# Optimization experiments

Hardware: AMD Instinct MI355X
Metric: run time of the kernel (lower is better)

## Reference

```python
import jax, jax.numpy as jnp
import numpy as np

ITERATIONS = 20
EPS = 1e-9

def setup_inputs() -> dict:
    key = jax.random.key(0)
    x = jax.random.normal(key, (8192, 64, 64), dtype=jnp.float32)
    return {"x": x}

def reference(x):
    M = jnp.exp(x)
    def body(_, M):
        M = M / (jnp.sum(M, axis=-1, keepdims=True) + EPS)
        M = M / (jnp.sum(M, axis=-2, keepdims=True) + EPS)
        return M
    M = jax.lax.fori_loop(0, ITERATIONS, body, M)
    return M
```

## Files before the change

kernel.cpp:

```cpp
#include <hip/hip_runtime.h>

#define ITERS 20
#define EPS 1e-9f

typedef float v2f __attribute__((ext_vector_type(2)));


template <int CTRL>
__device__ __forceinline__ float dpp_add(float x) {
    int yi = __builtin_amdgcn_update_dpp(0, __float_as_int(x), CTRL, 0xf, 0xf, true);
    return x + __int_as_float(yi);
}

#if __has_builtin(__builtin_amdgcn_permlane16_swap)
__device__ __forceinline__ float xadd16(float x) {
    unsigned u = __float_as_uint(x);
    auto r = __builtin_amdgcn_permlane16_swap(u, u, false, false);
    return __uint_as_float(r[0]) + __uint_as_float(r[1]);
}
#else
__device__ __forceinline__ float xadd16(float x) {
    return x + __int_as_float(__builtin_amdgcn_ds_swizzle(__float_as_int(x), 0x401F));
}
#endif

#if __has_builtin(__builtin_amdgcn_permlane32_swap)
__device__ __forceinline__ float xadd32(float x) {
    unsigned u = __float_as_uint(x);
    auto r = __builtin_amdgcn_permlane32_swap(u, u, false, false);
    return __uint_as_float(r[0]) + __uint_as_float(r[1]);
}
#else
__device__ __forceinline__ float xadd32(float x) {
    return x + __shfl_xor(x, 32, 64);
}
#endif

__device__ __forceinline__ v2f pk_mul(v2f a, v2f b) {
    v2f d;
    asm("v_pk_mul_f32 %0, %1, %2" : "=v"(d) : "v"(a), "v"(b));
    return d;
}
__device__ __forceinline__ v2f pk_fma(v2f a, v2f b, v2f c) {
    v2f d;
    asm("v_pk_fma_f32 %0, %1, %2, %3" : "=v"(d) : "v"(a), "v"(b), "v"(c));
    return d;
}
__device__ __forceinline__ v2f pk_add(v2f a, v2f b) {
    v2f d;
    asm("v_pk_add_f32 %0, %1, %2" : "=v"(d) : "v"(a), "v"(b));
    return d;
}
__device__ __forceinline__ v2f pk_fma_bl(v2f a, v2f u2, v2f c) {
    v2f d;
    asm("v_pk_fma_f32 %0, %1, %2, %3 op_sel:[0,0,0] op_sel_hi:[1,0,1]"
        : "=v"(d) : "v"(a), "v"(u2), "v"(c));
    return d;
}
__device__ __forceinline__ v2f pk_fma_bh(v2f a, v2f u2, v2f c) {
    v2f d;
    asm("v_pk_fma_f32 %0, %1, %2, %3 op_sel:[0,1,0] op_sel_hi:[1,1,1]"
        : "=v"(d) : "v"(a), "v"(u2), "v"(c));
    return d;
}
__device__ __forceinline__ v2f pk_mul_bl(v2f a, v2f u2) {
    v2f d;
    asm("v_pk_mul_f32 %0, %1, %2 op_sel:[0,0] op_sel_hi:[1,0]"
        : "=v"(d) : "v"(a), "v"(u2));
    return d;
}
__device__ __forceinline__ v2f pk_mul_bh(v2f a, v2f u2) {
    v2f d;
    asm("v_pk_mul_f32 %0, %1, %2 op_sel:[0,1] op_sel_hi:[1,1]"
        : "=v"(d) : "v"(a), "v"(u2));
    return d;
}

__global__ __launch_bounds__(256, 2) void sinkhorn_kernel(
        const float* __restrict__ x, float* __restrict__ out, int nmat) {
    const int lane = threadIdx.x & 63;
    const int wave = threadIdx.x >> 6;
    const int mat  = blockIdx.x * 4 + wave;
    if (mat >= nmat) return;
    const int bi = lane >> 3;
    const int bj = lane & 7;

    const float4* __restrict__ xin = (const float4*)(x + (size_t)mat * 4096);

    v2f b2[8][4];
    #pragma unroll
    for (int r = 0; r < 8; ++r) {
        float4 lo = xin[(8 * bi + r) * 16 + 2 * bj + 0];
        float4 hi = xin[(8 * bi + r) * 16 + 2 * bj + 1];
        b2[r][0] = (v2f){__expf(lo.x), __expf(lo.y)};
        b2[r][1] = (v2f){__expf(lo.z), __expf(lo.w)};
        b2[r][2] = (v2f){__expf(hi.x), __expf(hi.y)};
        b2[r][3] = (v2f){__expf(hi.z), __expf(hi.w)};
    }

    v2f uu2[4], vv2[4];
    #pragma unroll
    for (int i = 0; i < 4; ++i) {
        uu2[i] = (v2f){1.0f, 1.0f};
        vv2[i] = (v2f){1.0f, 1.0f};
    }

    for (int it = 0; it < ITERS; ++it) {
        float p[8];
        #pragma unroll
        for (int r = 0; r < 8; ++r) {
            v2f s2 = pk_mul(b2[r][0], vv2[0]);
            s2 = pk_fma(b2[r][1], vv2[1], s2);
            s2 = pk_fma(b2[r][2], vv2[2], s2);
            s2 = pk_fma(b2[r][3], vv2[3], s2);
            p[r] = s2.x + s2.y;
        }
        #pragma unroll
        for (int r = 0; r < 8; ++r) p[r] = dpp_add<0xB1>(p[r]);
        #pragma unroll
        for (int r = 0; r < 8; ++r) p[r] = dpp_add<0x4E>(p[r]);
        #pragma unroll
        for (int r = 0; r < 8; ++r) p[r] = dpp_add<0x141>(p[r]);
        #pragma unroll
        for (int k = 0; k < 4; ++k) {
            uu2[k].x = __builtin_amdgcn_rcpf(p[2 * k + 0] + EPS);
            uu2[k].y = __builtin_amdgcn_rcpf(p[2 * k + 1] + EPS);
        }

        v2f qe[4], qo[4];
        #pragma unroll
        for (int c = 0; c < 4; ++c) {
            qe[c] = pk_mul_bl(b2[0][c], uu2[0]);
            qo[c] = pk_mul_bh(b2[1][c], uu2[0]);
        }
        #pragma unroll
        for (int k = 1; k < 4; ++k) {
            #pragma unroll
            for (int c = 0; c < 4; ++c) {
                qe[c] = pk_fma_bl(b2[2 * k + 0][c], uu2[k], qe[c]);
                qo[c] = pk_fma_bh(b2[2 * k + 1][c], uu2[k], qo[c]);
            }
        }
        float q[8];
        #pragma unroll
        for (int c = 0; c < 4; ++c) {
            v2f s2 = pk_add(qe[c], qo[c]);
            q[2 * c + 0] = s2.x;
            q[2 * c + 1] = s2.y;
        }
        #pragma unroll
        for (int c = 0; c < 8; ++c) q[c] = dpp_add<0x128>(q[c]);
        #pragma unroll
        for (int c = 0; c < 8; ++c) q[c] = xadd16(q[c]);
        #pragma unroll
        for (int c = 0; c < 8; ++c) q[c] = xadd32(q[c]);
        #pragma unroll
        for (int c = 0; c < 4; ++c) {
            vv2[c].x = __builtin_amdgcn_rcpf(q[2 * c + 0] + EPS);
            vv2[c].y = __builtin_amdgcn_rcpf(q[2 * c + 1] + EPS);
        }
    }

    float4* __restrict__ o = (float4*)(out + (size_t)mat * 4096);
    #pragma unroll
    for (int r = 0; r < 8; ++r) {
        v2f u2 = (r & 1) ? (v2f){uu2[r >> 1].y, uu2[r >> 1].y}
                         : (v2f){uu2[r >> 1].x, uu2[r >> 1].x};
        v2f w0 = pk_mul(b2[r][0], pk_mul(vv2[0], u2));
        v2f w1 = pk_mul(b2[r][1], pk_mul(vv2[1], u2));
        v2f w2 = pk_mul(b2[r][2], pk_mul(vv2[2], u2));
        v2f w3 = pk_mul(b2[r][3], pk_mul(vv2[3], u2));
        float4 lo, hi;
        lo.x = w0.x; lo.y = w0.y; lo.z = w1.x; lo.w = w1.y;
        hi.x = w2.x; hi.y = w2.y; hi.z = w3.x; hi.w = w3.y;
        o[(8 * bi + r) * 16 + 2 * bj + 0] = lo;
        o[(8 * bi + r) * 16 + 2 * bj + 1] = hi;
    }
}

extern "C" void kernel_launch(void* const* d_in, const int* in_sizes, int n_in,
                              void* d_out, int out_size, void* d_ws, size_t ws_size,
                              hipStream_t stream) {
    const float* x = (const float*)d_in[0];
    float* out = (float*)d_out;
    const int nmat = in_sizes[0] / 4096;
    const int blocks = (nmat + 3) / 4;
    sinkhorn_kernel<<<blocks, 256, 0, stream>>>(x, out, nmat);
}
```

Baseline: 249.5 us.

## Process several matrices per wave with async global-to-LDS prefetch

Each wave now handles four consecutive matrices in turn. It prefetches the next matrix into a per-wave LDS buffer via global_load_lds while it runs the Sinkhorn iterations on the current one in registers. The block shrinks to 128 threads and the grid to a quarter of its former wave count, so per-wave load cost is paid only once up front. The catch is that far fewer waves stay resident per SIMD to hide the latency of the DPP/permlane reduction chains. The vmcnt(0) waits also serialize against the previous matrix's global stores.

```diff
diff --git a/kernel.cpp b/kernel.cpp
--- a/kernel.cpp
+++ b/kernel.cpp
@@ -2,8 +2,10 @@
 
 #define ITERS 20
 #define EPS 1e-9f
+#define MPW 4
 
 typedef float v2f __attribute__((ext_vector_type(2)));
+typedef unsigned int u32;
 
 
 template <int CTRL>
@@ -37,19 +39,13 @@
 #endif
 
 __device__ __forceinline__ v2f pk_mul(v2f a, v2f b) {
-    v2f d;
-    asm("v_pk_mul_f32 %0, %1, %2" : "=v"(d) : "v"(a), "v"(b));
-    return d;
+    v2f d; asm("v_pk_mul_f32 %0, %1, %2" : "=v"(d) : "v"(a), "v"(b)); return d;
 }
 __device__ __forceinline__ v2f pk_fma(v2f a, v2f b, v2f c) {
-    v2f d;
-    asm("v_pk_fma_f32 %0, %1, %2, %3" : "=v"(d) : "v"(a), "v"(b), "v"(c));
-    return d;
+    v2f d; asm("v_pk_fma_f32 %0, %1, %2, %3" : "=v"(d) : "v"(a), "v"(b), "v"(c)); return d;
 }
 __device__ __forceinline__ v2f pk_add(v2f a, v2f b) {
-    v2f d;
-    asm("v_pk_add_f32 %0, %1, %2" : "=v"(d) : "v"(a), "v"(b));
-    return d;
+    v2f d; asm("v_pk_add_f32 %0, %1, %2" : "=v"(d) : "v"(a), "v"(b)); return d;
 }
 __device__ __forceinline__ v2f pk_fma_bl(v2f a, v2f u2, v2f c) {
     v2f d;
@@ -76,105 +72,137 @@
     return d;
 }
 
-__global__ __launch_bounds__(256, 2) void sinkhorn_kernel(
+__device__ __forceinline__ void dma_mat(float* lds, const float* gsrc, int lane) {
+#if __has_builtin(__builtin_amdgcn_global_load_lds)
+    #pragma unroll
+    for (int k = 0; k < 16; ++k) {
+        __builtin_amdgcn_global_load_lds(
+            (const __attribute__((address_space(1))) u32*)(gsrc + k * 256 + lane * 4),
+            (__attribute__((address_space(3))) u32*)(lds + k * 256),
+            16, 0, 0);
+    }
+#else
+    #pragma unroll
+    for (int k = 0; k < 16; ++k)
+        ((float4*)lds)[k * 64 + lane] = ((const float4*)gsrc)[k * 64 + lane];
+#endif
+}
+
+__global__ __launch_bounds__(128, 2) void sinkhorn_kernel(
         const float* __restrict__ x, float* __restrict__ out, int nmat) {
+    __shared__ float lbuf[2][4096];
+
     const int lane = threadIdx.x & 63;
     const int wave = threadIdx.x >> 6;
-    const int mat  = blockIdx.x * 4 + wave;
-    if (mat >= nmat) return;
+    const int wid  = blockIdx.x * 2 + wave;
+    const int mat0 = wid * MPW;
+    if (mat0 >= nmat) return;
     const int bi = lane >> 3;
     const int bj = lane & 7;
-
-    const float4* __restrict__ xin = (const float4*)(x + (size_t)mat * 4096);
-
-    v2f b2[8][4];
-    #pragma unroll
-    for (int r = 0; r < 8; ++r) {
-        float4 lo = xin[(8 * bi + r) * 16 + 2 * bj + 0];
-        float4 hi = xin[(8 * bi + r) * 16 + 2 * bj + 1];
-        b2[r][0] = (v2f){__expf(lo.x), __expf(lo.y)};
-        b2[r][1] = (v2f){__expf(lo.z), __expf(lo.w)};
-        b2[r][2] = (v2f){__expf(hi.x), __expf(hi.y)};
-        b2[r][3] = (v2f){__expf(hi.z), __expf(hi.w)};
-    }
-
-    v2f uu2[4], vv2[4];
-    #pragma unroll
-    for (int i = 0; i < 4; ++i) {
-        uu2[i] = (v2f){1.0f, 1.0f};
-        vv2[i] = (v2f){1.0f, 1.0f};
-    }
-
-    for (int it = 0; it < ITERS; ++it) {
-        float p[8];
+    float* lw = lbuf[wave];
+
+    dma_mat(lw, x + (size_t)mat0 * 4096, lane);
+
+    for (int m = 0; m < MPW; ++m) {
+        const int mat = mat0 + m;
+        if (mat >= nmat) break;
+
+        asm volatile("s_waitcnt vmcnt(0)" ::: "memory");
+
+        v2f b2[8][4];
+        const float4* ls = (const float4*)lw;
         #pragma unroll
         for (int r = 0; r < 8; ++r) {
-            v2f s2 = pk_mul(b2[r][0], vv2[0]);
-            s2 = pk_fma(b2[r][1], vv2[1], s2);
-            s2 = pk_fma(b2[r][2], vv2[2], s2);
-            s2 = pk_fma(b2[r][3], vv2[3], s2);
-            p[r] = s2.x + s2.y;
-        }
+            float4 lo = ls[(8 * bi + r) * 16 + 2 * bj + 0];
+            float4 hi = ls[(8 * bi + r) * 16 + 2 * bj + 1];
+            b2[r][0] = (v2f){__expf(lo.x), __expf(lo.y)};
+            b2[r][1] = (v2f){__expf(lo.z), __expf(lo.w)};
+            b2[r][2] = (v2f){__expf(hi.x), __expf(hi.y)};
+            b2[r][3] = (v2f){__expf(hi.z), __expf(hi.w)};
+        }
+        asm volatile("s_waitcnt lgkmcnt(0)" ::: "memory");
+
+        if (m + 1 < MPW && mat + 1 < nmat)
+            dma_mat(lw, x + (size_t)(mat + 1) * 4096, lane);
+
+        v2f uu2[4], vv2[4];
         #pragma unroll
-        for (int r = 0; r < 8; ++r) p[r] = dpp_add<0xB1>(p[r]);
+        for (int i = 0; i < 4; ++i) {
+            uu2[i] = (v2f){1.0f, 1.0f};
+            vv2[i] = (v2f){1.0f, 1.0f};
+        }
+
+        for (int it = 0; it < ITERS; ++it) {
+            float p[8];
+            #pragma unroll
+            for (int r = 0; r < 8; ++r) {
+                v2f s2 = pk_mul(b2[r][0], vv2[0]);
+                s2 = pk_fma(b2[r][1], vv2[1], s2);
+                s2 = pk_fma(b2[r][2], vv2[2], s2);
+                s2 = pk_fma(b2[r][3], vv2[3], s2);
+                p[r] = s2.x + s2.y;
+            }
+            #pragma unroll
+            for (int r = 0; r < 8; ++r) p[r] = dpp_add<0xB1>(p[r]);
+            #pragma unroll
+            for (int r = 0; r < 8; ++r) p[r] = dpp_add<0x4E>(p[r]);
+            #pragma unroll
+            for (int r = 0; r < 8; ++r) p[r] = dpp_add<0x141>(p[r]);
+            #pragma unroll
+            for (int k = 0; k < 4; ++k) {
+                uu2[k].x = __builtin_amdgcn_rcpf(p[2 * k + 0] + EPS);
+                uu2[k].y = __builtin_amdgcn_rcpf(p[2 * k + 1] + EPS);
+            }
+
+            v2f qe[4], qo[4];
+            #pragma unroll
+            for (int c = 0; c < 4; ++c) {
+                qe[c] = pk_mul_bl(b2[0][c], uu2[0]);
+                qo[c] = pk_mul_bh(b2[1][c], uu2[0]);
+            }
+            #pragma unroll
+            for (int k = 1; k < 4; ++k) {
+                #pragma unroll
+                for (int c = 0; c < 4; ++c) {
+                    qe[c] = pk_fma_bl(b2[2 * k + 0][c], uu2[k], qe[c]);
+                    qo[c] = pk_fma_bh(b2[2 * k + 1][c], uu2[k], qo[c]);
+                }
+            }
+            float q[8];
+            #pragma unroll
+            for (int c = 0; c < 4; ++c) {
+                v2f s2 = pk_add(qe[c], qo[c]);
+                q[2 * c + 0] = s2.x;
+                q[2 * c + 1] = s2.y;
+            }
+            #pragma unroll
+            for (int c = 0; c < 8; ++c) q[c] = dpp_add<0x128>(q[c]);
+            #pragma unroll
+            for (int c = 0; c < 8; ++c) q[c] = xadd16(q[c]);
+            #pragma unroll
+            for (int c = 0; c < 8; ++c) q[c] = xadd32(q[c]);
+            #pragma unroll
+            for (int c = 0; c < 4; ++c) {
+                vv2[c].x = __builtin_amdgcn_rcpf(q[2 * c + 0] + EPS);
+                vv2[c].y = __builtin_amdgcn_rcpf(q[2 * c + 1] + EPS);
+            }
+        }
+
+        float4* __restrict__ o = (float4*)(out + (size_t)mat * 4096);
         #pragma unroll
-        for (int r = 0; r < 8; ++r) p[r] = dpp_add<0x4E>(p[r]);
-        #pragma unroll
-        for (int r = 0; r < 8; ++r) p[r] = dpp_add<0x141>(p[r]);
-        #pragma unroll
-        for (int k = 0; k < 4; ++k) {
-            uu2[k].x = __builtin_amdgcn_rcpf(p[2 * k + 0] + EPS);
-            uu2[k].y = __builtin_amdgcn_rcpf(p[2 * k + 1] + EPS);
-        }
-
-        v2f qe[4], qo[4];
-        #pragma unroll
-        for (int c = 0; c < 4; ++c) {
-            qe[c] = pk_mul_bl(b2[0][c], uu2[0]);
-            qo[c] = pk_mul_bh(b2[1][c], uu2[0]);
-        }
-        #pragma unroll
-        for (int k = 1; k < 4; ++k) {
-            #pragma unroll
-            for (int c = 0; c < 4; ++c) {
-                qe[c] = pk_fma_bl(b2[2 * k + 0][c], uu2[k], qe[c]);
-                qo[c] = pk_fma_bh(b2[2 * k + 1][c], uu2[k], qo[c]);
-            }
-        }
-        float q[8];
-        #pragma unroll
-        for (int c = 0; c < 4; ++c) {
-            v2f s2 = pk_add(qe[c], qo[c]);
-            q[2 * c + 0] = s2.x;
-            q[2 * c + 1] = s2.y;
-        }
-        #pragma unroll
-        for (int c = 0; c < 8; ++c) q[c] = dpp_add<0x128>(q[c]);
-        #pragma unroll
-        for (int c = 0; c < 8; ++c) q[c] = xadd16(q[c]);
-        #pragma unroll
-        for (int c = 0; c < 8; ++c) q[c] = xadd32(q[c]);
-        #pragma unroll
-        for (int c = 0; c < 4; ++c) {
-            vv2[c].x = __builtin_amdgcn_rcpf(q[2 * c + 0] + EPS);
-            vv2[c].y = __builtin_amdgcn_rcpf(q[2 * c + 1] + EPS);
-        }
-    }
-
-    float4* __restrict__ o = (float4*)(out + (size_t)mat * 4096);
-    #pragma unroll
-    for (int r = 0; r < 8; ++r) {
-        v2f u2 = (r & 1) ? (v2f){uu2[r >> 1].y, uu2[r >> 1].y}
-                         : (v2f){uu2[r >> 1].x, uu2[r >> 1].x};
-        v2f w0 = pk_mul(b2[r][0], pk_mul(vv2[0], u2));
-        v2f w1 = pk_mul(b2[r][1], pk_mul(vv2[1], u2));
-        v2f w2 = pk_mul(b2[r][2], pk_mul(vv2[2], u2));
-        v2f w3 = pk_mul(b2[r][3], pk_mul(vv2[3], u2));
-        float4 lo, hi;
-        lo.x = w0.x; lo.y = w0.y; lo.z = w1.x; lo.w = w1.y;
-        hi.x = w2.x; hi.y = w2.y; hi.z = w3.x; hi.w = w3.y;
-        o[(8 * bi + r) * 16 + 2 * bj + 0] = lo;
-        o[(8 * bi + r) * 16 + 2 * bj + 1] = hi;
+        for (int r = 0; r < 8; ++r) {
+            v2f u2 = (r & 1) ? (v2f){uu2[r >> 1].y, uu2[r >> 1].y}
+                             : (v2f){uu2[r >> 1].x, uu2[r >> 1].x};
+            v2f w0 = pk_mul(b2[r][0], pk_mul(vv2[0], u2));
+            v2f w1 = pk_mul(b2[r][1], pk_mul(vv2[1], u2));
+            v2f w2 = pk_mul(b2[r][2], pk_mul(vv2[2], u2));
+            v2f w3 = pk_mul(b2[r][3], pk_mul(vv2[3], u2));
+            float4 lo, hi;
+            lo.x = w0.x; lo.y = w0.y; lo.z = w1.x; lo.w = w1.y;
+            hi.x = w2.x; hi.y = w2.y; hi.z = w3.x; hi.w = w3.y;
+            o[(8 * bi + r) * 16 + 2 * bj + 0] = lo;
+            o[(8 * bi + r) * 16 + 2 * bj + 1] = hi;
+        }
     }
 }
 
@@ -184,6 +212,6 @@
     const float* x = (const float*)d_in[0];
     float* out = (float*)d_out;
     const int nmat = in_sizes[0] / 4096;
-    const int blocks = (nmat + 3) / 4;
-    sinkhorn_kernel<<<blocks, 256, 0, stream>>>(x, out, nmat);
-}
+    const int blocks = (nmat + 2 * MPW - 1) / (2 * MPW);
+    sinkhorn_kernel<<<blocks, 128, 0, stream>>>(x, out, nmat);
+}
```

Measured after the change: 262.0 us. +5.0%, slower.
